# Kernel tuning notes

Hardware: AMD Instinct MI355X
Metric: run time of the kernel (lower is better)

The kernel has to match this reference:

```python
import jax, jax.numpy as jnp
import numpy as np

N = 10000   # nodes
E = 160000  # edges (before self-loops)
IN = 77     # input feature dim
H = 4       # heads (layers 1,2)
C = 128     # per-head out channels


def setup_inputs() -> dict:
    key = jax.random.key(0)
    ks = jax.random.split(key, 16)
    p = lambda k, shape: (jax.random.normal(k, shape, jnp.float32) * 0.1)
    z = lambda n: jnp.zeros((n,), jnp.float32)
    return {
        "x": jax.random.normal(ks[0], (N, IN), jnp.float32),
        "edge_index": jax.random.randint(ks[1], (2, E), 0, N),
        # layer 1: 77 -> H*C
        "Wl1": p(ks[2], (H * C, IN)), "bl1": z(H * C),
        "Wr1": p(ks[3], (H * C, IN)), "br1": z(H * C),
        "att1": p(ks[4], (H, C)), "b1": z(H * C),
        # layer 2: H*C -> H*C
        "Wl2": p(ks[5], (H * C, H * C)), "bl2": z(H * C),
        "Wr2": p(ks[6], (H * C, H * C)), "br2": z(H * C),
        "att2": p(ks[7], (H, C)), "b2": z(H * C),
        # layer 3: H*C -> C (1 head)
        "Wl3": p(ks[8], (C, H * C)), "bl3": z(C),
        "Wr3": p(ks[9], (C, H * C)), "br3": z(C),
        "att3": p(ks[10], (1, C)), "b3": z(C),
    }


def _gatv2_layer(x, src, dst, Wl, bl, Wr, br, att, bias, heads, outc):
    """PyG GATv2Conv (eval mode, self-loops already in src/dst, concat=True)."""
    n = x.shape[0]
    xl = (x @ Wl.T + bl).reshape(n, heads, outc)  # source transform
    xr = (x @ Wr.T + br).reshape(n, heads, outc)  # target transform
    # edge-wise score: a^T LeakyReLU(xl[src] + xr[dst])
    e = jax.nn.leaky_relu(xl[src] + xr[dst], negative_slope=0.2)  # [E,H,C]
    logits = jnp.einsum('ehc,hc->eh', e, att)                      # [E,H]
    # segment softmax over edges grouped by destination node
    m = jax.lax.stop_gradient(jax.ops.segment_max(logits, dst, num_segments=n))
    ev = jnp.exp(logits - m[dst])
    denom = jax.ops.segment_sum(ev, dst, num_segments=n)
    alpha = ev / (denom[dst] + 1e-16)                              # [E,H]
    # scatter-add weighted messages
    out = jax.ops.segment_sum(xl[src] * alpha[:, :, None], dst, num_segments=n)
    return out.reshape(n, heads * outc) + bias


def reference(x, edge_index, Wl1, bl1, Wr1, br1, att1, b1,
              Wl2, bl2, Wr2, br2, att2, b2,
              Wl3, bl3, Wr3, br3, att3, b3):
    n = x.shape[0]
    loop = jnp.arange(n)
    src = jnp.concatenate([edge_index[0], loop])  # add self-loops (PyG default)
    dst = jnp.concatenate([edge_index[1], loop])
    h = jax.nn.elu(_gatv2_layer(x, src, dst, Wl1, bl1, Wr1, br1, att1, b1, H, C))
    h = jax.nn.elu(_gatv2_layer(h, src, dst, Wl2, bl2, Wr2, br2, att2, b2, H, C))
    return _gatv2_layer(h, src, dst, Wl3, bl3, Wr3, br3, att3, b3, 1, C)
```

## Files before the change

kernel.cpp:

```cpp
#include <hip/hip_runtime.h>
#include <hip/hip_bf16.h>
#include <math.h>

typedef __attribute__((ext_vector_type(8))) short short8;
typedef __attribute__((ext_vector_type(4))) float f32x4;
typedef __attribute__((ext_vector_type(2))) float f32x2;
typedef __attribute__((ext_vector_type(4))) unsigned int u32x4;

__device__ __forceinline__ f32x2 pk_add(f32x2 a, f32x2 b) {
  f32x2 d; asm("v_pk_add_f32 %0, %1, %2" : "=v"(d) : "v"(a), "v"(b)); return d;
}
__device__ __forceinline__ f32x2 pk_fma(f32x2 a, f32x2 b, f32x2 c) {
  f32x2 d; asm("v_pk_fma_f32 %0, %1, %2, %3" : "=v"(d) : "v"(a), "v"(b), "v"(c)); return d;
}
__device__ __forceinline__ f32x2 pk_abs(f32x2 a) {
  union { f32x2 f; unsigned int u[2]; } x; x.f = a;
  x.u[0] &= 0x7fffffffu; x.u[1] &= 0x7fffffffu;
  return x.f;
}
__device__ __forceinline__ f32x2 unpk(unsigned int w) {
  union { f32x2 f; unsigned int u[2]; } x;
  x.u[0] = w << 16;
  x.u[1] = w & 0xffff0000u;
  return x.f;
}

template <int CTRL>
__device__ __forceinline__ float dpp_add(float x) {
  int y = __builtin_amdgcn_update_dpp(0, __builtin_bit_cast(int, x), CTRL, 0xF, 0xF, true);
  return x + __builtin_bit_cast(float, y);
}
__device__ __forceinline__ float row16_sum(float p) {
  p = dpp_add<0xB1>(p);
  p = dpp_add<0x4E>(p);
  p = dpp_add<0x124>(p);
  p = dpp_add<0x128>(p);
  return p;
}

__device__ __forceinline__ void load_lds16(const void* g, void* l) {
  __builtin_amdgcn_global_load_lds(
      (const __attribute__((address_space(1))) unsigned int*)g,
      (__attribute__((address_space(3))) unsigned int*)l, 16, 0, 0);
}

__global__ __launch_bounds__(256) void gemm_mfma(
    const __hip_bfloat16* __restrict__ A, const __hip_bfloat16* __restrict__ B,
    const float* __restrict__ bl, const float* __restrict__ br, int halfN,
    __hip_bfloat16* __restrict__ out, int M, int K, int Nout) {
  __shared__ __hip_bfloat16 As[128 * 32];
  __shared__ __hip_bfloat16 Bs[128 * 32];
  int t = threadIdx.x;
  int w = t >> 6, l = t & 63;
  int lr = l & 15, lh = l >> 4;
  int wr = w >> 1, wc = w & 1;
  int m0 = blockIdx.y * 128, n0 = blockIdx.x * 128;
  f32x4 acc[4][4] = {};
  int nk = K >> 5;
  for (int ks = 0; ks < nk; ++ks) {
    int k0 = ks << 5;
#pragma unroll
    for (int p = 0; p < 2; ++p) {
      int c = p * 256 + t;
      int row = c >> 2, sub = c & 3;
      int gm = m0 + row; if (gm >= M) gm = M - 1;
      const __hip_bfloat16* gsrc = A + (size_t)gm * K + k0 + sub * 8;
      char* ldst = (char*)As + (size_t)(p * 256 + w * 64) * 16;
      load_lds16(gsrc, ldst);
    }
#pragma unroll
    for (int p = 0; p < 2; ++p) {
      int c = p * 256 + t;
      int row = c >> 2, sub = c & 3;
      const __hip_bfloat16* gsrc = B + (size_t)(n0 + row) * K + k0 + sub * 8;
      char* ldst = (char*)Bs + (size_t)(p * 256 + w * 64) * 16;
      load_lds16(gsrc, ldst);
    }
    __syncthreads();
    short8 af[4], bf[4];
#pragma unroll
    for (int mt = 0; mt < 4; ++mt)
      af[mt] = *(const short8*)(As + (size_t)(wr * 64 + mt * 16 + lr) * 32 + lh * 8);
#pragma unroll
    for (int nt = 0; nt < 4; ++nt)
      bf[nt] = *(const short8*)(Bs + (size_t)(wc * 64 + nt * 16 + lr) * 32 + lh * 8);
#pragma unroll
    for (int mt = 0; mt < 4; ++mt)
#pragma unroll
      for (int nt = 0; nt < 4; ++nt)
        acc[mt][nt] = __builtin_amdgcn_mfma_f32_16x16x32_bf16(af[mt], bf[nt], acc[mt][nt], 0, 0, 0);
    __syncthreads();
  }
#pragma unroll
  for (int mt = 0; mt < 4; ++mt) {
#pragma unroll
    for (int r = 0; r < 4; ++r) {
      int gm = m0 + wr * 64 + mt * 16 + lh * 4 + r;
      if (gm >= M) continue;
#pragma unroll
      for (int nt = 0; nt < 4; ++nt) {
        int gn = n0 + wc * 64 + nt * 16 + lr;
        float bv = (gn < halfN) ? bl[gn] : br[gn - halfN];
        out[(size_t)gm * Nout + gn] = __float2bfloat16(acc[mt][nt][r] + bv);
      }
    }
  }
}

struct CastSeg { const float* src; __hip_bfloat16* dst; int rows, K, Kp, row0, start; };
struct CastArgs { CastSeg s[7]; int total; };

__global__ __launch_bounds__(256) void k_prep(CastArgs A, const int* __restrict__ ei,
                                              int E, int N, int* __restrict__ deg) {
  int stride = gridDim.x * blockDim.x;
  int tid0 = blockIdx.x * blockDim.x + threadIdx.x;
  for (int i = tid0; i < A.total; i += stride) {
    int si = 0;
#pragma unroll
    for (int j = 1; j < 7; j++) if (i >= A.s[j].start) si = j;
    CastSeg sg = A.s[si];
    int li = i - sg.start;
    int r = li / sg.Kp, k = li - r * sg.Kp;
    float v = (k < sg.K) ? sg.src[(size_t)r * sg.K + k] : 0.f;
    sg.dst[(size_t)(sg.row0 + r) * sg.Kp + k] = __float2bfloat16(v);
  }
  int ET = E + N;
  for (int e = tid0; e < ET; e += stride) {
    int d = (e < E) ? ei[E + e] : (e - E);
    atomicAdd(&deg[d], 1);
  }
}

__global__ __launch_bounds__(256) void k_scan_perm(const int* __restrict__ deg, int N,
                                                   int* __restrict__ rp, int* __restrict__ cursor,
                                                   int* __restrict__ perm) {
  __shared__ int part[256];
  __shared__ int bcnt[64];
  __shared__ int boff[64];
  int t = threadIdx.x;
  int chunk = (N + 255) / 256;
  int lo = t * chunk;
  int hi = lo + chunk; if (hi > N) hi = N;
  int s = 0;
  for (int i = lo; i < hi; ++i) s += deg[i];
  part[t] = s;
  if (t < 64) bcnt[t] = 0;
  __syncthreads();
  for (int off = 1; off < 256; off <<= 1) {
    int x = (t >= off) ? part[t - off] : 0;
    __syncthreads();
    part[t] += x;
    __syncthreads();
  }
  int run = (t == 0) ? 0 : part[t - 1];
  for (int i = lo; i < hi; ++i) {
    rp[i] = run;
    cursor[i] = run;
    run += deg[i];
    int b = deg[i] < 63 ? deg[i] : 63;
    atomicAdd(&bcnt[b], 1);
  }
  if (t == 255) rp[N] = run;
  __syncthreads();
  if (t == 0) {
    int acc = 0;
    for (int b = 63; b >= 0; --b) { boff[b] = acc; acc += bcnt[b]; }
  }
  __syncthreads();
  for (int i = lo; i < hi; ++i) {
    int b = deg[i] < 63 ? deg[i] : 63;
    int pos = atomicAdd(&boff[b], 1);
    perm[pos] = i;
  }
}

__global__ void k_scatter(const int* __restrict__ ei, int E, int N,
                          int* __restrict__ cursor, int* __restrict__ srcs) {
  int e = blockIdx.x * blockDim.x + threadIdx.x;
  int ET = E + N;
  if (e >= ET) {
    if (e < ET + 64) srcs[e] = 0;
    return;
  }
  int s = (e < E) ? ei[e] : (e - E);
  int d = (e < E) ? ei[E + e] : (e - E);
  int pos = atomicAdd(&cursor[d], 1);
  srcs[pos] = s;
}

__global__ __launch_bounds__(256) void k_edge2(
    const __hip_bfloat16* __restrict__ xl, const __hip_bfloat16* __restrict__ xr,
    const int* __restrict__ rp, const int* __restrict__ srcs,
    const int* __restrict__ perm, const float* __restrict__ att,
    const float* __restrict__ bias, int N, __hip_bfloat16* __restrict__ out) {
  const int LD = 1024;
  int lane = threadIdx.x & 63;
  int hl = lane & 31;
  bool hi = lane >= 32;
  int nw = (blockIdx.x * blockDim.x + threadIdx.x) >> 6;
  if (nw >= N) return;
  int n = __builtin_amdgcn_readfirstlane(perm[nw]);

  f32x2 a06[8], a04[8], xrv2[8];
#pragma unroll
  for (int p = 0; p < 8; ++p) {
    float alo = att[hl * 16 + 2 * p], ahi = att[hl * 16 + 2 * p + 1];
    a06[p].x = 0.6f * alo; a06[p].y = 0.6f * ahi;
    a04[p].x = 0.4f * alo; a04[p].y = 0.4f * ahi;
  }
  {
    const unsigned int* xw = (const unsigned int*)(xr + (size_t)n * LD + hl * 16);
#pragma unroll
    for (int p = 0; p < 8; ++p) xrv2[p] = unpk(xw[p]);
  }

  int s0 = __builtin_amdgcn_readfirstlane(rp[n]);
  int s1 = __builtin_amdgcn_readfirstlane(rp[n + 1]);
  int len = s1 - s0;
  int lenA = (len + 1) >> 1;
  int lenB = len - lenA;
  int iA = s0, iB = s0 + lenA;

  float sum = 0.f;
  f32x2 acc2[8];
#pragma unroll
  for (int p = 0; p < 8; ++p) { acc2[p].x = 0.f; acc2[p].y = 0.f; }

  auto rowPtr = [&](int sA, int sB) -> const u32x4* {
    int s = hi ? sB : sA;
    return (const u32x4*)(xl + (size_t)s * LD + hl * 16);
  };

  u32x4 curLo, curHi;
  {
    const u32x4* p = rowPtr(srcs[iA], srcs[iB]);
    curLo = p[0]; curHi = p[1];
  }
  for (int t = 0; t < lenA; ++t) {
    const u32x4* pn = rowPtr(srcs[iA + t + 1], srcs[iB + t + 1]);
    u32x4 nLo = pn[0], nHi = pn[1];
    f32x2 xv2[8], p2; p2.x = 0.f; p2.y = 0.f;
#pragma unroll
    for (int p = 0; p < 8; ++p) {
      unsigned int wv = (p < 4) ? curLo[p & 3] : curHi[p & 3];
      xv2[p] = unpk(wv);
      f32x2 s = pk_add(xv2[p], xrv2[p]);
      f32x2 sa = pk_abs(s);
      p2 = pk_fma(a06[p], s, p2);
      p2 = pk_fma(a04[p], sa, p2);
    }
    float pp = p2.x + p2.y;
    pp = dpp_add<0xB1>(pp);
    pp = dpp_add<0x4E>(pp);
    pp += __shfl_xor(pp, 4, 64);
    float wgt = __expf(pp);
    if (hi && t >= lenB) wgt = 0.f;
    sum += wgt;
    f32x2 w2; w2.x = wgt; w2.y = wgt;
#pragma unroll
    for (int p = 0; p < 8; ++p) acc2[p] = pk_fma(w2, xv2[p], acc2[p]);
    curLo = nLo; curHi = nHi;
  }

  sum += __shfl_xor(sum, 32, 64);
#pragma unroll
  for (int p = 0; p < 8; ++p) {
    f32x2 o;
    o.x = __shfl_xor(acc2[p].x, 32, 64);
    o.y = __shfl_xor(acc2[p].y, 32, 64);
    acc2[p] = pk_add(acc2[p], o);
  }
  float inv = 1.f / (sum + 1e-16f);
  int cbase = hl * 16 + (hi ? 8 : 0);
  short8 o;
#pragma unroll
  for (int q = 0; q < 4; ++q) {
    f32x2 v = hi ? acc2[4 + q] : acc2[q];
    float r0 = v.x * inv + bias[cbase + 2 * q];
    float r1 = v.y * inv + bias[cbase + 2 * q + 1];
    r0 = r0 > 0.f ? r0 : expm1f(r0);
    r1 = r1 > 0.f ? r1 : expm1f(r1);
    __hip_bfloat16 b0 = __float2bfloat16(r0);
    __hip_bfloat16 b1 = __float2bfloat16(r1);
    o[2 * q] = __builtin_bit_cast(short, b0);
    o[2 * q + 1] = __builtin_bit_cast(short, b1);
  }
  *(short8*)(out + (size_t)n * 512 + cbase) = o;
}

__global__ __launch_bounds__(256) void k_edge4(
    const __hip_bfloat16* __restrict__ xl, const __hip_bfloat16* __restrict__ xr,
    const int* __restrict__ rp, const int* __restrict__ srcs,
    const int* __restrict__ perm, const float* __restrict__ att,
    const float* __restrict__ bias, int N, float* __restrict__ out) {
  const int LD = 256;
  int lane = threadIdx.x & 63;
  int hl = lane & 15;
  int g = lane >> 4;
  int nw = (blockIdx.x * blockDim.x + threadIdx.x) >> 6;
  if (nw >= N) return;
  int n = __builtin_amdgcn_readfirstlane(perm[nw]);

  f32x2 a06[4], a04[4], xrv2[4];
#pragma unroll
  for (int p = 0; p < 4; ++p) {
    float alo = att[hl * 8 + 2 * p], ahi = att[hl * 8 + 2 * p + 1];
    a06[p].x = 0.6f * alo; a06[p].y = 0.6f * ahi;
    a04[p].x = 0.4f * alo; a04[p].y = 0.4f * ahi;
  }
  {
    const unsigned int* xw = (const unsigned int*)(xr + (size_t)n * LD + hl * 8);
#pragma unroll
    for (int p = 0; p < 4; ++p) xrv2[p] = unpk(xw[p]);
  }

  int s0 = __builtin_amdgcn_readfirstlane(rp[n]);
  int s1 = __builtin_amdgcn_readfirstlane(rp[n + 1]);
  int len = s1 - s0;
  int base = len >> 2, rem = len & 3;
  int l0 = base + (rem > 0 ? 1 : 0);
  int l1 = base + (rem > 1 ? 1 : 0);
  int l2 = base + (rem > 2 ? 1 : 0);
  int st0 = 0, st1 = l0, st2 = l0 + l1, st3 = l0 + l1 + l2;
  int lg = base + ((g < rem) ? 1 : 0);
  int itmax = (len < 4) ? 1 : l0;
  if (l0 == 0) itmax = 0;

  float sum = 0.f;
  f32x2 acc2[4];
#pragma unroll
  for (int p = 0; p < 4; ++p) { acc2[p].x = 0.f; acc2[p].y = 0.f; }

  auto rowPtr = [&](int e0, int e1, int e2, int e3) -> const u32x4* {
    int s = (g == 0) ? e0 : (g == 1) ? e1 : (g == 2) ? e2 : e3;
    return (const u32x4*)(xl + (size_t)s * LD + hl * 8);
  };

  u32x4 cur = *rowPtr(srcs[s0 + st0], srcs[s0 + st1], srcs[s0 + st2], srcs[s0 + st3]);
  for (int t = 0; t < itmax; ++t) {
    u32x4 nxt = *rowPtr(srcs[s0 + st0 + t + 1], srcs[s0 + st1 + t + 1],
                        srcs[s0 + st2 + t + 1], srcs[s0 + st3 + t + 1]);
    f32x2 xv2[4], p2; p2.x = 0.f; p2.y = 0.f;
#pragma unroll
    for (int p = 0; p < 4; ++p) {
      xv2[p] = unpk(cur[p]);
      f32x2 s = pk_add(xv2[p], xrv2[p]);
      f32x2 sa = pk_abs(s);
      p2 = pk_fma(a06[p], s, p2);
      p2 = pk_fma(a04[p], sa, p2);
    }
    float pp = p2.x + p2.y;
    pp = row16_sum(pp);
    float wgt = (t < lg) ? __expf(pp) : 0.f;
    sum += wgt;
    f32x2 w2; w2.x = wgt; w2.y = wgt;
#pragma unroll
    for (int p = 0; p < 4; ++p) acc2[p] = pk_fma(w2, xv2[p], acc2[p]);
    cur = nxt;
  }

  sum += __shfl_xor(sum, 16, 64);
  sum += __shfl_xor(sum, 32, 64);
#pragma unroll
  for (int p = 0; p < 4; ++p) {
    acc2[p].x += __shfl_xor(acc2[p].x, 16, 64);
    acc2[p].y += __shfl_xor(acc2[p].y, 16, 64);
    acc2[p].x += __shfl_xor(acc2[p].x, 32, 64);
    acc2[p].y += __shfl_xor(acc2[p].y, 32, 64);
  }
  float inv = 1.f / (sum + 1e-16f);
  f32x2 v = (g == 0) ? acc2[0] : (g == 1) ? acc2[1] : (g == 2) ? acc2[2] : acc2[3];
  int cb = hl * 8 + 2 * g;
  f32x2 r;
  r.x = v.x * inv + bias[cb];
  r.y = v.y * inv + bias[cb + 1];
  *(f32x2*)(out + (size_t)n * 128 + cb) = r;
}

extern "C" void kernel_launch(void* const* d_in, const int* in_sizes, int n_in,
                              void* d_out, int out_size, void* d_ws, size_t ws_size,
                              hipStream_t stream) {
  const int IN = 77, Kp1 = 96, Hh = 4, Cc = 128, HC = Hh * Cc;
  const int N = in_sizes[0] / IN;
  const int E = in_sizes[1] / 2;
  const int ET = E + N;

  const float* x   = (const float*)d_in[0];
  const int*   ei  = (const int*)d_in[1];
  const float* Wl1 = (const float*)d_in[2];  const float* bl1 = (const float*)d_in[3];
  const float* Wr1 = (const float*)d_in[4];  const float* br1 = (const float*)d_in[5];
  const float* att1= (const float*)d_in[6];  const float* b1  = (const float*)d_in[7];
  const float* Wl2 = (const float*)d_in[8];  const float* bl2 = (const float*)d_in[9];
  const float* Wr2 = (const float*)d_in[10]; const float* br2 = (const float*)d_in[11];
  const float* att2= (const float*)d_in[12]; const float* b2  = (const float*)d_in[13];
  const float* Wl3 = (const float*)d_in[14]; const float* bl3 = (const float*)d_in[15];
  const float* Wr3 = (const float*)d_in[16]; const float* br3 = (const float*)d_in[17];
  const float* att3= (const float*)d_in[18]; const float* b3  = (const float*)d_in[19];
  float* out = (float*)d_out;

  char* w = (char*)d_ws;
  size_t off = 0;
  auto alloc = [&](size_t bytes) -> void* {
    void* p = w + off;
    off += (bytes + 255) & ~(size_t)255;
    return p;
  };
  __hip_bfloat16* xlr = (__hip_bfloat16*)alloc((size_t)N * 2 * HC * 2);
  __hip_bfloat16* hb  = (__hip_bfloat16*)alloc((size_t)N * HC * 2);
  __hip_bfloat16* Wc1 = (__hip_bfloat16*)alloc((size_t)2 * HC * Kp1 * 2);
  __hip_bfloat16* Wc2 = (__hip_bfloat16*)alloc((size_t)2 * HC * HC * 2);
  __hip_bfloat16* Wc3 = (__hip_bfloat16*)alloc((size_t)2 * Cc * HC * 2);
  int*   deg    = (int*)alloc((size_t)N * 4);
  int*   rp     = (int*)alloc((size_t)(N + 1) * 4);
  int*   cursor = (int*)alloc((size_t)N * 4);
  int*   srcs   = (int*)alloc((size_t)(ET + 64) * 4);
  int*   perm   = (int*)alloc((size_t)N * 4);

  CastArgs CA;
  int cum = 0;
  auto seg = [&](int idx, const float* src, __hip_bfloat16* dst, int rows, int K, int Kp, int row0) {
    CA.s[idx] = {src, dst, rows, K, Kp, row0, cum};
    cum += rows * Kp;
  };
  seg(0, Wl1, Wc1, HC, IN, Kp1, 0);
  seg(1, Wr1, Wc1, HC, IN, Kp1, HC);
  seg(2, Wl2, Wc2, HC, HC, HC, 0);
  seg(3, Wr2, Wc2, HC, HC, HC, HC);
  seg(4, Wl3, Wc3, Cc, HC, HC, 0);
  seg(5, Wr3, Wc3, Cc, HC, HC, Cc);
  seg(6, x,   hb,  N,  IN, Kp1, 0);
  CA.total = cum;

  hipMemsetAsync(deg, 0, (size_t)N * 4, stream);
  k_prep<<<1024, 256, 0, stream>>>(CA, ei, E, N, deg);
  k_scan_perm<<<1, 256, 0, stream>>>(deg, N, rp, cursor, perm);
  k_scatter<<<(ET + 64 + 255) / 256, 256, 0, stream>>>(ei, E, N, cursor, srcs);

  int nodeBlocks = (N + 3) / 4;
  int mb = (N + 127) / 128;

  {
    dim3 g(2 * HC / 128, mb);
    gemm_mfma<<<g, 256, 0, stream>>>(hb, Wc1, bl1, br1, HC, xlr, N, Kp1, 2 * HC);
    k_edge2<<<nodeBlocks, 256, 0, stream>>>(xlr, xlr + HC, rp, srcs, perm, att1, b1, N, hb);
  }
  {
    dim3 g(2 * HC / 128, mb);
    gemm_mfma<<<g, 256, 0, stream>>>(hb, Wc2, bl2, br2, HC, xlr, N, HC, 2 * HC);
    k_edge2<<<nodeBlocks, 256, 0, stream>>>(xlr, xlr + HC, rp, srcs, perm, att2, b2, N, hb);
  }
  {
    dim3 g(2 * Cc / 128, mb);
    gemm_mfma<<<g, 256, 0, stream>>>(hb, Wc3, bl3, br3, Cc, xlr, N, HC, 2 * Cc);
    k_edge4<<<nodeBlocks, 256, 0, stream>>>(xlr, xlr + Cc, rp, srcs, perm, att3, b3, N, out);
  }
}
```

Before: 194.5 us.

## Remap GEMM workgroups per XCD, deepen gather prefetch, use 32-bit row offsets

```diff
diff --git a/kernel.cpp b/kernel.cpp
--- a/kernel.cpp
+++ b/kernel.cpp
@@ -50,11 +50,19 @@
     __hip_bfloat16* __restrict__ out, int M, int K, int Nout) {
   __shared__ __hip_bfloat16 As[128 * 32];
   __shared__ __hip_bfloat16 Bs[128 * 32];
+  int gx = gridDim.x;
+  int nwg = gx * gridDim.y;
+  int lid = blockIdx.y * gx + blockIdx.x;
+  int q = nwg >> 3, r = nwg & 7;
+  int xcd = lid & 7, li = lid >> 3;
+  int wgid = (xcd < r ? xcd * (q + 1) : r * (q + 1) + (xcd - r) * q) + li;
+  int bx = wgid % gx, by = wgid / gx;
+
   int t = threadIdx.x;
   int w = t >> 6, l = t & 63;
   int lr = l & 15, lh = l >> 4;
   int wr = w >> 1, wc = w & 1;
-  int m0 = blockIdx.y * 128, n0 = blockIdx.x * 128;
+  int m0 = by * 128, n0 = bx * 128;
   f32x4 acc[4][4] = {};
   int nk = K >> 5;
   for (int ks = 0; ks < nk; ++ks) {
@@ -94,14 +102,14 @@
 #pragma unroll
   for (int mt = 0; mt < 4; ++mt) {
 #pragma unroll
-    for (int r = 0; r < 4; ++r) {
-      int gm = m0 + wr * 64 + mt * 16 + lh * 4 + r;
+    for (int r2 = 0; r2 < 4; ++r2) {
+      int gm = m0 + wr * 64 + mt * 16 + lh * 4 + r2;
       if (gm >= M) continue;
 #pragma unroll
       for (int nt = 0; nt < 4; ++nt) {
         int gn = n0 + wc * 64 + nt * 16 + lr;
         float bv = (gn < halfN) ? bl[gn] : br[gn - halfN];
-        out[(size_t)gm * Nout + gn] = __float2bfloat16(acc[mt][nt][r] + bv);
+        out[(size_t)gm * Nout + gn] = __float2bfloat16(acc[mt][nt][r2] + bv);
       }
     }
   }
@@ -220,29 +228,30 @@
   int lenA = (len + 1) >> 1;
   int lenB = len - lenA;
   int iA = s0, iB = s0 + lenA;
+  unsigned laneOff = (unsigned)(hl * 32);
 
   float sum = 0.f;
   f32x2 acc2[8];
 #pragma unroll
   for (int p = 0; p < 8; ++p) { acc2[p].x = 0.f; acc2[p].y = 0.f; }
 
-  auto rowPtr = [&](int sA, int sB) -> const u32x4* {
-    int s = hi ? sB : sA;
-    return (const u32x4*)(xl + (size_t)s * LD + hl * 16);
+  auto loadPair = [&](int t, u32x4& lo, u32x4& hh) {
+    unsigned offA = ((unsigned)srcs[iA + t]) << 11;
+    unsigned offB = ((unsigned)srcs[iB + t]) << 11;
+    unsigned off = (hi ? offB : offA) + laneOff;
+    const u32x4* p = (const u32x4*)((const char*)xl + off);
+    lo = p[0]; hh = p[1];
   };
 
-  u32x4 curLo, curHi;
-  {
-    const u32x4* p = rowPtr(srcs[iA], srcs[iB]);
-    curLo = p[0]; curHi = p[1];
-  }
+  u32x4 lo0, hi0, lo1, hi1, lo2, hi2;
+  loadPair(0, lo0, hi0);
+  loadPair(1, lo1, hi1);
   for (int t = 0; t < lenA; ++t) {
-    const u32x4* pn = rowPtr(srcs[iA + t + 1], srcs[iB + t + 1]);
-    u32x4 nLo = pn[0], nHi = pn[1];
+    loadPair(t + 2, lo2, hi2);
     f32x2 xv2[8], p2; p2.x = 0.f; p2.y = 0.f;
 #pragma unroll
     for (int p = 0; p < 8; ++p) {
-      unsigned int wv = (p < 4) ? curLo[p & 3] : curHi[p & 3];
+      unsigned int wv = (p < 4) ? lo0[p & 3] : hi0[p & 3];
       xv2[p] = unpk(wv);
       f32x2 s = pk_add(xv2[p], xrv2[p]);
       f32x2 sa = pk_abs(s);
@@ -259,7 +268,7 @@
     f32x2 w2; w2.x = wgt; w2.y = wgt;
 #pragma unroll
     for (int p = 0; p < 8; ++p) acc2[p] = pk_fma(w2, xv2[p], acc2[p]);
-    curLo = nLo; curHi = nHi;
+    lo0 = lo1; hi0 = hi1; lo1 = lo2; hi1 = hi2;
   }
 
   sum += __shfl_xor(sum, 32, 64);
@@ -325,21 +334,25 @@
   int lg = base + ((g < rem) ? 1 : 0);
   int itmax = (len < 4) ? 1 : l0;
   if (l0 == 0) itmax = 0;
+  unsigned laneOff = (unsigned)(hl * 16);
 
   float sum = 0.f;
   f32x2 acc2[4];
 #pragma unroll
   for (int p = 0; p < 4; ++p) { acc2[p].x = 0.f; acc2[p].y = 0.f; }
 
-  auto rowPtr = [&](int e0, int e1, int e2, int e3) -> const u32x4* {
-    int s = (g == 0) ? e0 : (g == 1) ? e1 : (g == 2) ? e2 : e3;
-    return (const u32x4*)(xl + (size_t)s * LD + hl * 8);
+  auto loadRow = [&](int t) -> u32x4 {
+    unsigned o0 = ((unsigned)srcs[s0 + st0 + t]) << 9;
+    unsigned o1 = ((unsigned)srcs[s0 + st1 + t]) << 9;
+    unsigned o2 = ((unsigned)srcs[s0 + st2 + t]) << 9;
+    unsigned o3 = ((unsigned)srcs[s0 + st3 + t]) << 9;
+    unsigned off = ((g == 0) ? o0 : (g == 1) ? o1 : (g == 2) ? o2 : o3) + laneOff;
+    return *(const u32x4*)((const char*)xl + off);
   };
 
-  u32x4 cur = *rowPtr(srcs[s0 + st0], srcs[s0 + st1], srcs[s0 + st2], srcs[s0 + st3]);
+  u32x4 cur = loadRow(0);
   for (int t = 0; t < itmax; ++t) {
-    u32x4 nxt = *rowPtr(srcs[s0 + st0 + t + 1], srcs[s0 + st1 + t + 1],
-                        srcs[s0 + st2 + t + 1], srcs[s0 + st3 + t + 1]);
+    u32x4 nxt = loadRow(t + 1);
     f32x2 xv2[4], p2; p2.x = 0.f; p2.y = 0.f;
 #pragma unroll
     for (int p = 0; p < 4; ++p) {
```

Measured after the change: 192.7 us. No clear change (-1.0%).
